# Kernel tuning notes

Measured on AMD Instinct MI355X. Metric: run time of the kernel, lower is better.

## Reference

```python
import jax, jax.numpy as jnp
import numpy as np

FP8_E4M3_MAX = 448.0
BLOCK = 32
EPS = 1e-30


def _quantize_fp8(blocks):
    # blocks: (..., num_blocks, BLOCK) float32
    max_abs = jnp.max(jnp.abs(blocks), axis=-1)                      # (..., nb)
    scales = jnp.maximum(max_abs / FP8_E4M3_MAX, EPS)                # shared fp32 scale per block
    fp8 = (blocks / scales[..., None]).astype(jnp.float8_e4m3fn).astype(jnp.float32)
    return fp8, scales


def setup_inputs() -> dict:
    key = jax.random.key(0)
    k1, k2, k3 = jax.random.split(key, 3)
    x = jax.random.normal(k1, (2048, 2048), dtype=jnp.float32)
    weight = jax.random.normal(k2, (2048, 2048), dtype=jnp.float32) * 0.02
    bias = jax.random.normal(k3, (2048,), dtype=jnp.float32) * 0.02
    return {"x": x, "weight": weight, "bias": bias}


def reference(x, weight, bias):
    N, in_f = x.shape
    out_f = weight.shape[0]
    nb = in_f // BLOCK  # in_features is a multiple of BLOCK, so no padding needed

    x_fp8, x_scales = _quantize_fp8(x.reshape(N, nb, BLOCK))         # (N, nb, B), (N, nb)
    w_fp8, w_scales = _quantize_fp8(weight.reshape(out_f, nb, BLOCK))  # (out, nb, B), (out, nb)

    # per-block fp8-element dot products: (nb, N, out)
    elem_dots = jnp.einsum('nbk,jbk->bnj', x_fp8, w_fp8)
    # apply shared block scales and reduce over blocks: out[n,j] = sum_b sx[n,b]*sw[j,b]*dots[b,n,j]
    result = jnp.einsum('bnj,nb,jb->nj', elem_dots, x_scales, w_scales)
    return result + bias
```

## Files before the change

kernel.cpp:

```cpp
#include <hip/hip_runtime.h>
#include <hip/hip_bf16.h>


typedef __attribute__((ext_vector_type(8))) __bf16 bf16x8;
typedef __attribute__((ext_vector_type(4))) float f32x4;

#define NMAT 2048
#define ROWB 4096
#define FP8_MAX 448.0f

__device__ inline unsigned short bfbits(float f) {
  union { __hip_bfloat16 h; unsigned short u; } cv;
  cv.h = __float2bfloat16(f);
  return cv.u;
}

__device__ inline unsigned pack2(float a, float b, float scale) {
  int p = __builtin_amdgcn_cvt_pk_fp8_f32(a / scale, b / scale, 0, false);
  float qa = __builtin_amdgcn_cvt_f32_fp8(p, 0) * scale;
  float qb = __builtin_amdgcn_cvt_f32_fp8(p, 1) * scale;
  return (unsigned)bfbits(qa) | ((unsigned)bfbits(qb) << 16);
}

__global__ __launch_bounds__(256) void qdq_kernel(const float* __restrict__ in,
                                                  unsigned* __restrict__ out) {
  int b = blockIdx.x * 256 + threadIdx.x;
  const float4* p = (const float4*)(in + (size_t)b * 32);
  float4 v[8];
  float amax = 0.f;
#pragma unroll
  for (int i = 0; i < 8; ++i) {
    v[i] = p[i];
    amax = fmaxf(amax, fmaxf(fmaxf(fabsf(v[i].x), fabsf(v[i].y)),
                             fmaxf(fabsf(v[i].z), fabsf(v[i].w))));
  }
  float scale = fmaxf(amax / FP8_MAX, 1e-30f);
  unsigned r[16];
#pragma unroll
  for (int i = 0; i < 8; ++i) {
    r[2 * i]     = pack2(v[i].x, v[i].y, scale);
    r[2 * i + 1] = pack2(v[i].z, v[i].w, scale);
  }
  uint4* dst = (uint4*)(out + (size_t)b * 16);
  dst[0] = make_uint4(r[0], r[1], r[2], r[3]);
  dst[1] = make_uint4(r[4], r[5], r[6], r[7]);
  dst[2] = make_uint4(r[8], r[9], r[10], r[11]);
  dst[3] = make_uint4(r[12], r[13], r[14], r[15]);
}

__global__ __launch_bounds__(512) void gemm_kernel(const __bf16* __restrict__ A,
                                                   const __bf16* __restrict__ B,
                                                   const float* __restrict__ bias,
                                                   float* __restrict__ C) {
  __shared__ __align__(16) __bf16 As[128 * 32];
  __shared__ __align__(16) __bf16 Bs[128 * 32];
  const int tid  = threadIdx.x;
  const int lane = tid & 63;
  const int wid  = tid >> 6;
  const int wr   = wid >> 2;
  const int wc   = wid & 3;
  const int row0 = blockIdx.y * 128;
  const int col0 = blockIdx.x * 128;

  const int o  = tid * 16;
  const int sr = o >> 6;
  const int sc = o & 63;
  const char* Ag = (const char*)A + (size_t)(row0 + sr) * ROWB + sc;
  const char* Bg = (const char*)B + (size_t)(col0 + sr) * ROWB + sc;
  char* Al = (char*)As + o;
  char* Bl = (char*)Bs + o;

  const int l15 = lane & 15;
  const int kg  = (lane >> 4) * 8;
  const __bf16* Ard = As + (wr * 64 + l15) * 32 + kg;
  const __bf16* Brd = Bs + (wc * 32 + l15) * 32 + kg;

  f32x4 acc[4][2] = {};

  for (int kt = 0; kt < 64; ++kt) {
    __syncthreads();
    __builtin_amdgcn_global_load_lds(
        (const __attribute__((address_space(1))) unsigned*)(Ag + kt * 64),
        (__attribute__((address_space(3))) unsigned*)Al, 16, 0, 0);
    __builtin_amdgcn_global_load_lds(
        (const __attribute__((address_space(1))) unsigned*)(Bg + kt * 64),
        (__attribute__((address_space(3))) unsigned*)Bl, 16, 0, 0);
    __syncthreads();
    bf16x8 af[4], bf[2];
#pragma unroll
    for (int m = 0; m < 4; ++m) af[m] = *(const bf16x8*)(Ard + m * 16 * 32);
#pragma unroll
    for (int n = 0; n < 2; ++n) bf[n] = *(const bf16x8*)(Brd + n * 16 * 32);
#pragma unroll
    for (int m = 0; m < 4; ++m)
#pragma unroll
      for (int n = 0; n < 2; ++n)
        acc[m][n] =
            __builtin_amdgcn_mfma_f32_16x16x32_bf16(af[m], bf[n], acc[m][n], 0, 0, 0);
  }

  const int rb = row0 + wr * 64 + (lane >> 4) * 4;
#pragma unroll
  for (int n = 0; n < 2; ++n) {
    const int j = col0 + wc * 32 + n * 16 + l15;
    const float bv = bias[j];
#pragma unroll
    for (int m = 0; m < 4; ++m) {
#pragma unroll
      for (int r = 0; r < 4; ++r) {
        C[(size_t)(rb + m * 16 + r) * NMAT + j] = acc[m][n][r] + bv;
      }
    }
  }
}

extern "C" void kernel_launch(void* const* d_in, const int* in_sizes, int n_in,
                              void* d_out, int out_size, void* d_ws, size_t ws_size,
                              hipStream_t stream) {
  const float* x  = (const float*)d_in[0];
  const float* w  = (const float*)d_in[1];
  const float* bs = (const float*)d_in[2];
  float* out = (float*)d_out;

  unsigned* xd = (unsigned*)d_ws;
  unsigned* wd = xd + (NMAT * NMAT / 2);

  qdq_kernel<<<dim3(NMAT * (NMAT / 32) / 256), dim3(256), 0, stream>>>(x, xd);
  qdq_kernel<<<dim3(NMAT * (NMAT / 32) / 256), dim3(256), 0, stream>>>(w, wd);

  dim3 grid(NMAT / 128, NMAT / 128);
  gemm_kernel<<<grid, dim3(512), 0, stream>>>((const __bf16*)xd, (const __bf16*)wd,
                                              bs, out);
}
```

Baseline: 125.1 us.

## Double-buffer GEMM K tiles with swizzled LDS and merge quantize kernels

The GEMM now stages 64-wide K tiles into two 32KB LDS buffers. Each buffer is filled via global_load_lds with an XOR swizzle on the column offset, and the load for the next tile is issued while the current one is computed. This halves the number of barriers and hides global-load latency, and the swizzle is meant to reduce LDS bank conflicts. The two quantize launches are merged into one kernel in which each thread handles 4 elements and the block max is taken with shuffles, giving coalesced loads and stores. The cost is more LDS per block (64KB), which may cut occupancy.

```diff
diff --git a/kernel.cpp b/kernel.cpp
--- a/kernel.cpp
+++ b/kernel.cpp
@@ -6,7 +6,6 @@
 typedef __attribute__((ext_vector_type(4))) float f32x4;
 
 #define NMAT 2048
-#define ROWB 4096
 #define FP8_MAX 448.0f
 
 __device__ inline unsigned short bfbits(float f) {
@@ -22,38 +21,34 @@
   return (unsigned)bfbits(qa) | ((unsigned)bfbits(qb) << 16);
 }
 
-__global__ __launch_bounds__(256) void qdq_kernel(const float* __restrict__ in,
-                                                  unsigned* __restrict__ out) {
-  int b = blockIdx.x * 256 + threadIdx.x;
-  const float4* p = (const float4*)(in + (size_t)b * 32);
-  float4 v[8];
-  float amax = 0.f;
-#pragma unroll
-  for (int i = 0; i < 8; ++i) {
-    v[i] = p[i];
-    amax = fmaxf(amax, fmaxf(fmaxf(fabsf(v[i].x), fabsf(v[i].y)),
-                             fmaxf(fabsf(v[i].z), fabsf(v[i].w))));
-  }
+__global__ __launch_bounds__(256) void qdq_kernel(const float* __restrict__ x,
+                                                  uint2* __restrict__ xo,
+                                                  const float* __restrict__ w,
+                                                  uint2* __restrict__ wo) {
+  int g = blockIdx.x;
+  const float* in;
+  uint2* out;
+  if (g >= 4096) { in = w; out = wo; g -= 4096; }
+  else           { in = x; out = xo; }
+  const int t = threadIdx.x;
+  const size_t base = (size_t)g * 1024;
+  float4 v = ((const float4*)(in + base))[t];
+  float amax = fmaxf(fmaxf(fabsf(v.x), fabsf(v.y)), fmaxf(fabsf(v.z), fabsf(v.w)));
+  amax = fmaxf(amax, __shfl_xor(amax, 1));
+  amax = fmaxf(amax, __shfl_xor(amax, 2));
+  amax = fmaxf(amax, __shfl_xor(amax, 4));
   float scale = fmaxf(amax / FP8_MAX, 1e-30f);
-  unsigned r[16];
-#pragma unroll
-  for (int i = 0; i < 8; ++i) {
-    r[2 * i]     = pack2(v[i].x, v[i].y, scale);
-    r[2 * i + 1] = pack2(v[i].z, v[i].w, scale);
-  }
-  uint4* dst = (uint4*)(out + (size_t)b * 16);
-  dst[0] = make_uint4(r[0], r[1], r[2], r[3]);
-  dst[1] = make_uint4(r[4], r[5], r[6], r[7]);
-  dst[2] = make_uint4(r[8], r[9], r[10], r[11]);
-  dst[3] = make_uint4(r[12], r[13], r[14], r[15]);
+  uint2 r;
+  r.x = pack2(v.x, v.y, scale);
+  r.y = pack2(v.z, v.w, scale);
+  out[base / 4 + t] = r;
 }
 
 __global__ __launch_bounds__(512) void gemm_kernel(const __bf16* __restrict__ A,
                                                    const __bf16* __restrict__ B,
                                                    const float* __restrict__ bias,
                                                    float* __restrict__ C) {
-  __shared__ __align__(16) __bf16 As[128 * 32];
-  __shared__ __align__(16) __bf16 Bs[128 * 32];
+  __shared__ __align__(16) char lds[65536];
   const int tid  = threadIdx.x;
   const int lane = tid & 63;
   const int wid  = tid >> 6;
@@ -62,42 +57,81 @@
   const int row0 = blockIdx.y * 128;
   const int col0 = blockIdx.x * 128;
 
-  const int o  = tid * 16;
-  const int sr = o >> 6;
-  const int sc = o & 63;
-  const char* Ag = (const char*)A + (size_t)(row0 + sr) * ROWB + sc;
-  const char* Bg = (const char*)B + (size_t)(col0 + sr) * ROWB + sc;
-  char* Al = (char*)As + o;
-  char* Bl = (char*)Bs + o;
+  const int oA0 = tid * 16;
+  const int oA1 = oA0 + 8192;
+  const int r0 = oA0 >> 7, r1 = oA1 >> 7;
+  const int c0 = (oA0 & 127) ^ ((r0 & 7) << 4);
+  const int c1 = (oA1 & 127) ^ ((r1 & 7) << 4);
+  const char* AgS0 = (const char*)A + (size_t)(row0 + r0) * 4096 + c0;
+  const char* AgS1 = (const char*)A + (size_t)(row0 + r1) * 4096 + c1;
+  const char* BgS0 = (const char*)B + (size_t)(col0 + r0) * 4096 + c0;
+  const char* BgS1 = (const char*)B + (size_t)(col0 + r1) * 4096 + c1;
+
+#define STAGE(buf, kt) do {                                                      \
+    const int kb = (kt) * 128;                                                   \
+    char* lb = lds + (buf) * 32768;                                              \
+    __builtin_amdgcn_global_load_lds(                                            \
+        (const __attribute__((address_space(1))) unsigned*)(AgS0 + kb),          \
+        (__attribute__((address_space(3))) unsigned*)(lb + oA0), 16, 0, 0);      \
+    __builtin_amdgcn_global_load_lds(                                            \
+        (const __attribute__((address_space(1))) unsigned*)(AgS1 + kb),          \
+        (__attribute__((address_space(3))) unsigned*)(lb + oA1), 16, 0, 0);      \
+    __builtin_amdgcn_global_load_lds(                                            \
+        (const __attribute__((address_space(1))) unsigned*)(BgS0 + kb),          \
+        (__attribute__((address_space(3))) unsigned*)(lb + 16384 + oA0), 16, 0, 0);\
+    __builtin_amdgcn_global_load_lds(                                            \
+        (const __attribute__((address_space(1))) unsigned*)(BgS1 + kb),          \
+        (__attribute__((address_space(3))) unsigned*)(lb + 16384 + oA1), 16, 0, 0);\
+  } while (0)
 
   const int l15 = lane & 15;
-  const int kg  = (lane >> 4) * 8;
-  const __bf16* Ard = As + (wr * 64 + l15) * 32 + kg;
-  const __bf16* Brd = Bs + (wc * 32 + l15) * 32 + kg;
+  const int q16 = (lane >> 4) * 16;
+  const int swz = (l15 & 7) << 4;
+  const int ck0 = q16 ^ swz;
+  const int ck1 = (64 + q16) ^ swz;
+  const int aRow = (wr * 64 + l15) * 128;
+  const int bRow = (wc * 32 + l15) * 128;
 
   f32x4 acc[4][2] = {};
 
-  for (int kt = 0; kt < 64; ++kt) {
-    __syncthreads();
-    __builtin_amdgcn_global_load_lds(
-        (const __attribute__((address_space(1))) unsigned*)(Ag + kt * 64),
-        (__attribute__((address_space(3))) unsigned*)Al, 16, 0, 0);
-    __builtin_amdgcn_global_load_lds(
-        (const __attribute__((address_space(1))) unsigned*)(Bg + kt * 64),
-        (__attribute__((address_space(3))) unsigned*)Bl, 16, 0, 0);
-    __syncthreads();
-    bf16x8 af[4], bf[2];
+  auto compute = [&](const int buf) {
+    const char* ab = lds + buf * 32768;
+    const char* bb = ab + 16384;
+    bf16x8 a0[4], a1[4], b0[2], b1[2];
 #pragma unroll
-    for (int m = 0; m < 4; ++m) af[m] = *(const bf16x8*)(Ard + m * 16 * 32);
+    for (int m = 0; m < 4; ++m) {
+      a0[m] = *(const bf16x8*)(ab + aRow + m * 2048 + ck0);
+      a1[m] = *(const bf16x8*)(ab + aRow + m * 2048 + ck1);
+    }
 #pragma unroll
-    for (int n = 0; n < 2; ++n) bf[n] = *(const bf16x8*)(Brd + n * 16 * 32);
+    for (int n = 0; n < 2; ++n) {
+      b0[n] = *(const bf16x8*)(bb + bRow + n * 2048 + ck0);
+      b1[n] = *(const bf16x8*)(bb + bRow + n * 2048 + ck1);
+    }
 #pragma unroll
     for (int m = 0; m < 4; ++m)
 #pragma unroll
-      for (int n = 0; n < 2; ++n)
-        acc[m][n] =
-            __builtin_amdgcn_mfma_f32_16x16x32_bf16(af[m], bf[n], acc[m][n], 0, 0, 0);
+      for (int n = 0; n < 2; ++n) {
+        acc[m][n] = __builtin_amdgcn_mfma_f32_16x16x32_bf16(a0[m], b0[n], acc[m][n], 0, 0, 0);
+        acc[m][n] = __builtin_amdgcn_mfma_f32_16x16x32_bf16(a1[m], b1[n], acc[m][n], 0, 0, 0);
+      }
+  };
+
+  STAGE(0, 0);
+  __syncthreads();
+#pragma unroll 1
+  for (int t = 0; t < 30; t += 2) {
+    STAGE(1, t + 1);
+    compute(0);
+    __syncthreads();
+    STAGE(0, t + 2);
+    compute(1);
+    __syncthreads();
   }
+  STAGE(1, 31);
+  compute(0);
+  __syncthreads();
+  compute(1);
 
   const int rb = row0 + wr * 64 + (lane >> 4) * 4;
 #pragma unroll
@@ -105,13 +139,12 @@
     const int j = col0 + wc * 32 + n * 16 + l15;
     const float bv = bias[j];
 #pragma unroll
-    for (int m = 0; m < 4; ++m) {
+    for (int m = 0; m < 4; ++m)
 #pragma unroll
-      for (int r = 0; r < 4; ++r) {
+      for (int r = 0; r < 4; ++r)
         C[(size_t)(rb + m * 16 + r) * NMAT + j] = acc[m][n][r] + bv;
-      }
-    }
   }
+#undef STAGE
 }
 
 extern "C" void kernel_launch(void* const* d_in, const int* in_sizes, int n_in,
@@ -122,11 +155,10 @@
   const float* bs = (const float*)d_in[2];
   float* out = (float*)d_out;
 
-  unsigned* xd = (unsigned*)d_ws;
-  unsigned* wd = xd + (NMAT * NMAT / 2);
+  uint2* xd = (uint2*)d_ws;
+  uint2* wd = xd + (NMAT * (size_t)NMAT / 4);
 
-  qdq_kernel<<<dim3(NMAT * (NMAT / 32) / 256), dim3(256), 0, stream>>>(x, xd);
-  qdq_kernel<<<dim3(NMAT * (NMAT / 32) / 256), dim3(256), 0, stream>>>(w, wd);
+  qdq_kernel<<<dim3(8192), dim3(256), 0, stream>>>(x, xd, w, wd);
 
   dim3 grid(NMAT / 128, NMAT / 128);
   gemm_kernel<<<grid, dim3(512), 0, stream>>>((const __bf16*)xd, (const __bf16*)wd,
```

Measured after the change: 107.3 us. -14.2%, faster.
